# Performance work log

Hardware: AMD Instinct MI355X
Metric: run time of the kernel (lower is better)

## Reference

```python
import jax, jax.numpy as jnp
import numpy as np

NEG = -1e30  # stand-in for -inf, safe for grads


def ctc_loss(log_probs, targets, input_lengths, target_lengths):
    """PyTorch-style CTC loss, blank=0, reduction='mean'.
    log_probs: [B, T, V] log-softmaxed; targets: [B, S] (values in [1, V)).
    """
    B, T, V = log_probs.shape
    S = targets.shape[1]
    L = 2 * S + 1  # extended label seq: blank-interleaved
    ext = jnp.zeros((B, L), jnp.int32).at[:, 1::2].set(targets.astype(jnp.int32))
    prev2 = jnp.pad(ext[:, :-2], ((0, 0), (2, 0)), constant_values=-1)
    skip = (ext != 0) & (ext != prev2)  # [B, L] allow alpha[l-2] transition
    barange = jnp.arange(B)[:, None]

    # t = 0 init
    lp0e = log_probs[:, 0, :][barange, ext]  # [B, L]
    alpha0 = jnp.full((B, L), NEG, log_probs.dtype)
    alpha0 = alpha0.at[:, 0].set(lp0e[:, 0]).at[:, 1].set(lp0e[:, 1])

    def step(alpha, xs):
        t, lp_t = xs  # lp_t: [B, V]
        lpe = lp_t[barange, ext]  # [B, L]
        a1 = jnp.pad(alpha[:, :-1], ((0, 0), (1, 0)), constant_values=NEG)
        a2 = jnp.pad(alpha[:, :-2], ((0, 0), (2, 0)), constant_values=NEG)
        a2 = jnp.where(skip, a2, NEG)
        new = lpe + jnp.logaddexp(jnp.logaddexp(alpha, a1), a2)
        # freeze alpha past each sequence's length
        new = jnp.where((t < input_lengths)[:, None], new, alpha)
        return new, None

    ts = jnp.arange(1, T)
    lps = jnp.swapaxes(log_probs, 0, 1)[1:]  # [T-1, B, V]
    alpha, _ = jax.lax.scan(step, alpha0, (ts, lps))

    tl = target_lengths.astype(jnp.int32)
    brange = jnp.arange(B)
    end = alpha[brange, 2 * tl]       # trailing blank
    end2 = alpha[brange, 2 * tl - 1]  # last label
    per = -jnp.logaddexp(end, end2)
    # reduction='mean': divide each loss by its target_length, then batch mean
    return jnp.mean(per / target_lengths.astype(per.dtype))


def setup_inputs() -> dict:
    key = jax.random.key(0)
    k1, k2, k3 = jax.random.split(key, 3)
    B, T, Fd, V, S = 32, 2048, 1024, 256, 256
    features = jax.random.normal(k1, (B, T, Fd), jnp.float32)
    W = jax.random.normal(k2, (V, Fd), jnp.float32) / np.sqrt(Fd)
    b = jnp.zeros((V,), jnp.float32)
    targets = jax.random.randint(k3, (B, S), 1, V)  # avoid blank=0
    input_lengths = jnp.full((B,), T, jnp.int32)
    target_lengths = jnp.full((B,), S, jnp.int32)
    return {"features": features, "W": W, "b": b, "targets": targets,
            "input_lengths": input_lengths, "target_lengths": target_lengths}


def reference(features, W, b, targets, input_lengths, target_lengths):
    # dropout is identity at inference; classifier then log_softmax in fp32
    logits = jnp.einsum('btf,vf->btv', features, W) + b
    log_probs = jax.nn.log_softmax(logits.astype(jnp.float32), axis=-1)
    return ctc_loss(log_probs, targets, input_lengths, target_lengths)
```

## Files before the change

kernel.cpp:

```cpp
#include <hip/hip_runtime.h>
#include <hip/hip_bf16.h>

using bf16x8 = __attribute__((ext_vector_type(8))) short;
using f32x4  = __attribute__((ext_vector_type(4))) float;

constexpr int Bn = 32;
constexpr int Tn = 2048;
constexpr int Fn = 1024;
constexpr int Vn = 256;
constexpr int Sn = 256;
constexpr int Ln = 2 * Sn + 1;
constexpr int Mn = Bn * Tn;
constexpr int G2P = 272;
constexpr int DQ = 16;
constexpr int ABP = 520;

#define NEGF (-1e30f)

__device__ __forceinline__ float exp2fast(float x) { return __builtin_amdgcn_exp2f(x); }
__device__ __forceinline__ float log2fast(float x) { return __builtin_amdgcn_logf(x); }

__device__ __forceinline__ unsigned int cvt_pk_bf16(float lo, float hi) {
    unsigned int r;
    asm("v_cvt_pk_bf16_f32 %0, %1, %2" : "=v"(r) : "v"(lo), "v"(hi));
    return r;
}

__device__ __forceinline__ float lae2(float x, float y) {
    float m = fmaxf(x, y);
    float d = fminf(x, y) - m;
    return m + log2fast(1.0f + exp2fast(d));
}
__device__ __forceinline__ float lae3(float x, float y, float z) {
    float m  = fmaxf(fmaxf(x, y), z);
    float md = __builtin_amdgcn_fmed3f(x, y, z);
    float mn = fminf(fminf(x, y), z);
    return m + log2fast(1.0f + exp2fast(md - m) + exp2fast(mn - m));
}

__global__ __launch_bounds__(256) void wcvt(const float* __restrict__ W,
                                            unsigned short* __restrict__ Wb)
{
    const int idx = (blockIdx.x * 256 + threadIdx.x) * 4;
    float4 v = *reinterpret_cast<const float4*>(W + idx);
    uint2 p;
    p.x = cvt_pk_bf16(v.x, v.y);
    p.y = cvt_pk_bf16(v.z, v.w);
    *reinterpret_cast<uint2*>(Wb + idx) = p;
}

__global__ __launch_bounds__(512, 4) void gemm_ctc(
    const float* __restrict__ A,
    const unsigned short* __restrict__ Wb,
    const float* __restrict__ bias,
    const int* __restrict__ targets,
    float* __restrict__ G2)
{
    __shared__ char smem[81920];
    unsigned short* sA = (unsigned short*)smem;
    unsigned short* sB = (unsigned short*)(smem + 16384);
    float* yL    = (float*)smem;
    float* sRedA = (float*)(smem + 66048);
    float* sRedB = (float*)(smem + 68096);

    const int tid  = threadIdx.x;
    const int wid  = tid >> 6, lane = tid & 63;
    const int quad = lane >> 4, c16 = lane & 15;
    const int m0 = blockIdx.x * 128;
    const int wm = (wid & 1) * 64;
    const int wn = (wid >> 1) * 64;

    f32x4 acc[4][4] = {};

    const int arow = tid >> 2;
    const int akq  = (tid & 3) << 4;
    const float* aPtr = A + (size_t)(m0 + arow) * Fn + akq;
    const int aswz = (arow & 7) << 4;
    char* sAbase = (char*)sA + arow * 128;
    const int ab0 = (akq * 2) ^ aswz;
    const int ab1 = (akq * 2 + 16) ^ aswz;

    const int wrow8 = lane >> 3;
    const int wcol  = ((lane & 7) << 4) ^ (wrow8 << 4);

#define ISSUE_W(K0, BUF)                                                        \
    _Pragma("unroll")                                                           \
    for (int i = 0; i < 4; ++i) {                                               \
        const int rbase = wid * 32 + i * 8;                                     \
        const unsigned short* g = Wb + (size_t)(rbase + wrow8) * Fn + (K0);     \
        __builtin_amdgcn_global_load_lds(                                       \
            (const __attribute__((address_space(1))) unsigned int*)((const char*)g + wcol), \
            (__attribute__((address_space(3))) unsigned int*)((char*)sB + (BUF) * 32768 + rbase * 128), \
            16, 0, 0);                                                          \
    }

    ISSUE_W(0, 0);
    {
        const float4* ap = reinterpret_cast<const float4*>(aPtr);
        float4 av0 = ap[0], av1 = ap[1], av2 = ap[2], av3 = ap[3];
        uint4 p;
        p.x = cvt_pk_bf16(av0.x, av0.y); p.y = cvt_pk_bf16(av0.z, av0.w);
        p.z = cvt_pk_bf16(av1.x, av1.y); p.w = cvt_pk_bf16(av1.z, av1.w);
        *reinterpret_cast<uint4*>(sAbase + ab0) = p;
        p.x = cvt_pk_bf16(av2.x, av2.y); p.y = cvt_pk_bf16(av2.z, av2.w);
        p.z = cvt_pk_bf16(av3.x, av3.y); p.w = cvt_pk_bf16(av3.z, av3.w);
        *reinterpret_cast<uint4*>(sAbase + ab1) = p;
    }
    __syncthreads();

    for (int it = 0; it < 16; ++it) {
        float4 an0, an1, an2, an3;
        if (it < 15) {
            ISSUE_W((it + 1) * 64, (it + 1) & 1);
            const float4* ap = reinterpret_cast<const float4*>(aPtr + (it + 1) * 64);
            an0 = ap[0]; an1 = ap[1]; an2 = ap[2]; an3 = ap[3];
        }
        const char* sBb = (const char*)sB + (it & 1) * 32768;
        #pragma unroll
        for (int kh = 0; kh < 2; ++kh) {
            const int colq = kh * 64 + quad * 16;
            bf16x8 af[4], bf[4];
            #pragma unroll
            for (int mt = 0; mt < 4; ++mt) {
                const int r = wm + mt * 16 + c16;
                af[mt] = *reinterpret_cast<const bf16x8*>((const char*)sA + r * 128 + (colq ^ ((r & 7) << 4)));
            }
            #pragma unroll
            for (int nt = 0; nt < 4; ++nt) {
                const int r = wn + nt * 16 + c16;
                bf[nt] = *reinterpret_cast<const bf16x8*>(sBb + r * 128 + (colq ^ ((r & 7) << 4)));
            }
            #pragma unroll
            for (int mt = 0; mt < 4; ++mt)
                #pragma unroll
                for (int nt = 0; nt < 4; ++nt)
                    acc[mt][nt] = __builtin_amdgcn_mfma_f32_16x16x32_bf16(af[mt], bf[nt], acc[mt][nt], 0, 0, 0);
        }
        __syncthreads();
        if (it < 15) {
            uint4 p;
            p.x = cvt_pk_bf16(an0.x, an0.y); p.y = cvt_pk_bf16(an0.z, an0.w);
            p.z = cvt_pk_bf16(an1.x, an1.y); p.w = cvt_pk_bf16(an1.z, an1.w);
            *reinterpret_cast<uint4*>(sAbase + ab0) = p;
            p.x = cvt_pk_bf16(an2.x, an2.y); p.y = cvt_pk_bf16(an2.z, an2.w);
            p.z = cvt_pk_bf16(an3.x, an3.y); p.w = cvt_pk_bf16(an3.z, an3.w);
            *reinterpret_cast<uint4*>(sAbase + ab1) = p;
            __syncthreads();
        }
    }
#undef ISSUE_W

    const float L2E = 1.4426950408889634f;
    const int wng = wid >> 1;

    float bv[4];
    #pragma unroll
    for (int nt = 0; nt < 4; ++nt) bv[nt] = bias[wn + nt * 16 + c16];
    #pragma unroll
    for (int mt = 0; mt < 4; ++mt)
        #pragma unroll
        for (int nt = 0; nt < 4; ++nt)
            #pragma unroll
            for (int r = 0; r < 4; ++r)
                acc[mt][nt][r] += bv[nt];

    float rmx[4][4];
    #pragma unroll
    for (int mt = 0; mt < 4; ++mt)
        #pragma unroll
        for (int r = 0; r < 4; ++r) {
            float m = fmaxf(fmaxf(acc[mt][0][r], acc[mt][1][r]),
                            fmaxf(acc[mt][2][r], acc[mt][3][r]));
            #pragma unroll
            for (int off = 8; off >= 1; off >>= 1) m = fmaxf(m, __shfl_xor(m, off, 64));
            rmx[mt][r] = m;
        }
    __syncthreads();
    if (c16 == 0) {
        #pragma unroll
        for (int mt = 0; mt < 4; ++mt)
            #pragma unroll
            for (int r = 0; r < 4; ++r)
                sRedA[(wm + mt * 16 + quad * 4 + r) * 4 + wng] = rmx[mt][r];
    }
    __syncthreads();

    float mL[4][4], sm[4][4];
    #pragma unroll
    for (int mt = 0; mt < 4; ++mt)
        #pragma unroll
        for (int r = 0; r < 4; ++r) {
            const int row = wm + mt * 16 + quad * 4 + r;
            float4 mp = ((const float4*)sRedA)[row];
            mL[mt][r] = fmaxf(fmaxf(mp.x, mp.y), fmaxf(mp.z, mp.w)) * L2E;
            float s = 0.0f;
            #pragma unroll
            for (int nt = 0; nt < 4; ++nt)
                s += exp2fast(fmaf(acc[mt][nt][r], L2E, -mL[mt][r]));
            #pragma unroll
            for (int off = 8; off >= 1; off >>= 1) s += __shfl_xor(s, off, 64);
            sm[mt][r] = s;
        }
    if (c16 == 0) {
        #pragma unroll
        for (int mt = 0; mt < 4; ++mt)
            #pragma unroll
            for (int r = 0; r < 4; ++r)
                sRedB[(wm + mt * 16 + quad * 4 + r) * 4 + wng] = sm[mt][r];
    }
    __syncthreads();

    float cr[4][4];
    #pragma unroll
    for (int mt = 0; mt < 4; ++mt)
        #pragma unroll
        for (int r = 0; r < 4; ++r) {
            const int row = wm + mt * 16 + quad * 4 + r;
            float4 sp = ((const float4*)sRedB)[row];
            cr[mt][r] = -(mL[mt][r] + log2fast((sp.x + sp.y) + (sp.z + sp.w)));
        }

    const int* tg = targets + (m0 >> 11) * Sn;
    int tgc[5];
    #pragma unroll
    for (int k = 0; k < 5; ++k) {
        const int c = lane + (k << 6);
        tgc[k] = (c == 0) ? 0 : ((c < 257) ? tg[c - 1] : 0);
    }

    #pragma unroll
    for (int h = 0; h < 2; ++h) {
        if ((wid & 1) == h) {
            #pragma unroll
            for (int mt = 0; mt < 4; ++mt)
                #pragma unroll
                for (int nt = 0; nt < 4; ++nt)
                    #pragma unroll
                    for (int r = 0; r < 4; ++r)
                        yL[(mt * 16 + quad * 4 + r) * 258 + wn + nt * 16 + c16] =
                            fmaf(acc[mt][nt][r], L2E, cr[mt][r]);
        }
        __syncthreads();
        #pragma unroll
        for (int rr = 0; rr < 8; ++rr) {
            const int row = wid * 8 + rr;
            const float* yrow = yL + row * 258;
            float vals[5];
            #pragma unroll
            for (int k = 0; k < 5; ++k) vals[k] = yrow[tgc[k]];
            float* gout = G2 + (size_t)(m0 + h * 64 + row) * G2P;
            #pragma unroll
            for (int k = 0; k < 4; ++k) gout[lane + (k << 6)] = vals[k];
            if (lane == 0) gout[256] = vals[4];
        }
        __syncthreads();
    }
}

__global__ __launch_bounds__(512) void ctc_fb(
    const float* __restrict__ G2, const int* __restrict__ targets,
    const int* __restrict__ ilen, const int* __restrict__ tlen,
    float* __restrict__ abuf)
{
    const int blk = blockIdx.x;
    const bool bwd = blk >= Bn;
    const int b = bwd ? blk - Bn : blk;
    const int tid = threadIdx.x;
    const int w = tid >> 6, j = tid & 63;
    __shared__ float sAl[Ln];
    const float* __restrict__ Gb = G2 + (size_t)b * Tn * G2P;
    const int* tg = targets + b * Sn;
    const int len = ilen[b];
    const int tl  = tlen[b];
    float* outp = abuf + (size_t)(bwd ? Bn + b : b) * ABP;
    const int NEGI = __float_as_int(NEGF);

    if (!bwd) {
        const int own_lo = (w == 0) ? 0 : 64 * w + 2;
        const int own_hi = min(64 * w + 66, Ln);
        const int lbase  = 64 * w - 62 + 2 * j;
        const int l0 = lbase, l1 = lbase + 1;
        const int s_c = min(max(32 * w - 31 + j, 0), Sn - 1);

        const bool own0 = (l0 >= own_lo) && (l0 < own_hi);
        const bool own1 = (l1 >= own_lo) && (l1 < own_hi);
        const bool re0  = (l0 >= 0) && (l0 < Ln) && !own0;
        const bool re1  = (l1 >= 0) && (l1 < Ln) && !own1;
        bool sk1 = false;
        if (l1 >= 1 && l1 < Ln) { int s = l1 >> 1; sk1 = (s == 0) || (tg[s] != tg[s - 1]); }

        float a0, a1;
        {
            float bl0 = Gb[0];
            float od0 = Gb[1 + s_c];
            a0 = (l0 == 0) ? bl0 : NEGF;
            a1 = (l1 == 1) ? od0 : NEGF;
        }
        if (own0) sAl[l0] = a0;
        if (own1) sAl[l1] = a1;
        __syncthreads();
        if (re0) a0 = sAl[l0];
        if (re1) a1 = sAl[l1];
        __syncthreads();

        unsigned oB = G2P, oO = G2P + 1 + s_c;
        float plB[DQ], plO[DQ];
        #pragma unroll
        for (int d = 0; d < DQ; ++d) {
            plB[d] = Gb[oB]; plO[d] = Gb[oO];
            oB += G2P; oO += G2P;
        }

        int t = 1;
        for (int chunk = 0; chunk < 32; ++chunk) {
            #pragma unroll
            for (int kk = 0; kk < 32; ++kk, ++t) {
                const int pidx = kk & (DQ - 1);
                float gb = plB[pidx], go = plO[pidx];
                plB[pidx] = Gb[oB]; plO[pidx] = Gb[oO];
                oB += G2P; oO += G2P;
                float p = __int_as_float(__builtin_amdgcn_update_dpp(
                    NEGI, __float_as_int(a1), 0x138, 0xf, 0xf, false));
                if (t < len) {
                    float z  = sk1 ? p : NEGF;
                    float n0 = gb + lae2(a0, p);
                    float n1 = go + lae3(a1, a0, z);
                    a0 = n0; a1 = n1;
                }
            }
            if (own0) sAl[l0] = a0;
            if (own1) sAl[l1] = a1;
            __syncthreads();
            if (re0) a0 = sAl[l0];
            if (re1) a1 = sAl[l1];
            __syncthreads();
        }
        if (own0) outp[l0] = a0;
        if (own1) outp[l1] = a1;
    } else {
        const int l0 = 64 * w + 2 * j;
        const int l1 = l0 + 1;
        const int s  = 32 * w + j;
        const int s_c = min(s, Sn - 1);
        const bool act0 = l0 < Ln, act1 = l1 < Ln;
        const bool own0 = act0 && ((j < 32) || (l0 == Ln - 1));
        const bool own1 = act1 && (j < 32);
        const bool re0 = act0 && !own0, re1 = act1 && !own1;
        bool skb = false;
        if (s + 1 < Sn) skb = (tg[s + 1] != tg[s]);

        float a0 = (act0 && l0 == 2 * tl)     ? 0.0f : NEGF;
        float a1 = (act1 && l1 == 2 * tl - 1) ? 0.0f : NEGF;
        if (own0) sAl[l0] = a0;
        if (own1) sAl[l1] = a1;
        __syncthreads();
        if (re0) a0 = sAl[l0];
        if (re1) a1 = sAl[l1];
        __syncthreads();

        unsigned oB = (unsigned)Tn * G2P;
        unsigned oO = oB + 1 + s_c;
        float plB[DQ], plO[DQ];
        #pragma unroll
        for (int d = 0; d < DQ; ++d) {
            plB[d] = Gb[oB]; plO[d] = Gb[oO];
            oB -= G2P; oO -= G2P;
        }

        int tt = Tn;
        for (int chunk = 0; chunk < 32; ++chunk) {
            #pragma unroll
            for (int kk = 0; kk < 32; ++kk, --tt) {
                const int pidx = kk & (DQ - 1);
                float gb = plB[pidx], go = plO[pidx];
                plB[pidx] = Gb[oB]; plO[pidx] = Gb[oO];
                oB -= G2P; oO -= G2P;
                if (tt < len) {
                    float c0 = gb + a0;
                    float c1 = go + a1;
                    float d0 = __int_as_float(__builtin_amdgcn_update_dpp(
                        NEGI, __float_as_int(c0), 0x130, 0xf, 0xf, false));
                    float d1 = __int_as_float(__builtin_amdgcn_update_dpp(
                        NEGI, __float_as_int(c1), 0x130, 0xf, 0xf, false));
                    a0 = lae2(c0, c1);
                    a1 = lae3(c1, d0, skb ? d1 : NEGF);
                }
            }
            if (own0) sAl[l0] = a0;
            if (own1) sAl[l1] = a1;
            __syncthreads();
            if (re0) a0 = sAl[l0];
            if (re1) a1 = sAl[l1];
            __syncthreads();
        }
        if (own0) outp[l0] = a0;
        if (own1) outp[l1] = a1;
    }
}

__global__ __launch_bounds__(64) void ctc_combine(
    const float* __restrict__ abuf, const int* __restrict__ tlen,
    float* __restrict__ loss_b)
{
    const int b = blockIdx.x, lane = threadIdx.x;
    const float* ap = abuf + (size_t)b * ABP;
    const float* bp = abuf + (size_t)(Bn + b) * ABP;
    float x[9];
    #pragma unroll
    for (int k = 0; k < 9; ++k) {
        const int l = lane + (k << 6);
        x[k] = (l < Ln) ? (ap[l] + bp[l]) : NEGF;
    }
    float m = x[0];
    #pragma unroll
    for (int k = 1; k < 9; ++k) m = fmaxf(m, x[k]);
    #pragma unroll
    for (int off = 32; off >= 1; off >>= 1) m = fmaxf(m, __shfl_xor(m, off, 64));
    float s = 0.0f;
    #pragma unroll
    for (int k = 0; k < 9; ++k) s += exp2fast(x[k] - m);
    #pragma unroll
    for (int off = 32; off >= 1; off >>= 1) s += __shfl_xor(s, off, 64);
    if (lane == 0)
        loss_b[b] = -0.6931471805599453f * (m + log2fast(s)) / (float)tlen[b];
}

__global__ void final_reduce(const float* __restrict__ loss_b, float* __restrict__ out)
{
    const int lane = threadIdx.x;
    float v = (lane < Bn) ? loss_b[lane] : 0.0f;
    #pragma unroll
    for (int off = 32; off >= 1; off >>= 1) v += __shfl_xor(v, off, 64);
    if (lane == 0) out[0] = v * (1.0f / Bn);
}

extern "C" void kernel_launch(void* const* d_in, const int* in_sizes, int n_in,
                              void* d_out, int out_size, void* d_ws, size_t ws_size,
                              hipStream_t stream) {
    const float* feat = (const float*)d_in[0];
    const float* W    = (const float*)d_in[1];
    const float* bias = (const float*)d_in[2];
    const int* tgt    = (const int*)d_in[3];
    const int* il     = (const int*)d_in[4];
    const int* tl     = (const int*)d_in[5];
    float* out = (float*)d_out;

    char* ws = (char*)d_ws;
    float* G2 = (float*)ws;
    size_t g2b = (size_t)Mn * G2P * sizeof(float) + 32768;
    unsigned short* Wb = (unsigned short*)(ws + g2b);
    float* abuf  = (float*)(ws + g2b + (size_t)Vn * Fn * sizeof(unsigned short));
    float* lossb = abuf + 2 * Bn * ABP;

    wcvt<<<(Vn * Fn) / 1024, 256, 0, stream>>>(W, Wb);
    gemm_ctc<<<Mn / 128, 512, 0, stream>>>(feat, Wb, bias, tgt, G2);
    ctc_fb<<<2 * Bn, 512, 0, stream>>>(G2, tgt, il, tl, abuf);
    ctc_combine<<<Bn, 64, 0, stream>>>(abuf, tl, lossb);
    final_reduce<<<1, 64, 0, stream>>>(lossb, out);
}
```

Baseline: 564.4 us.

## Deepen GEMM prefetch to two stages with manual waitcnt and barriers

Result: no change. 562.1 us (-0.4%).

```diff
diff --git a/kernel.cpp b/kernel.cpp
--- a/kernel.cpp
+++ b/kernel.cpp
@@ -94,28 +94,40 @@
             16, 0, 0);                                                          \
     }
 
+#define LOAD_A(DST, K0) {                                                       \
+        const float4* ap = reinterpret_cast<const float4*>(aPtr + (K0));        \
+        DST[0] = ap[0]; DST[1] = ap[1]; DST[2] = ap[2]; DST[3] = ap[3]; }
+
+#define STORE_A(av) { uint4 p;                                                  \
+        p.x = cvt_pk_bf16(av[0].x, av[0].y); p.y = cvt_pk_bf16(av[0].z, av[0].w); \
+        p.z = cvt_pk_bf16(av[1].x, av[1].y); p.w = cvt_pk_bf16(av[1].z, av[1].w); \
+        *reinterpret_cast<uint4*>(sAbase + ab0) = p;                            \
+        p.x = cvt_pk_bf16(av[2].x, av[2].y); p.y = cvt_pk_bf16(av[2].z, av[2].w); \
+        p.z = cvt_pk_bf16(av[3].x, av[3].y); p.w = cvt_pk_bf16(av[3].z, av[3].w); \
+        *reinterpret_cast<uint4*>(sAbase + ab1) = p; }
+
+#define FENCE() asm volatile("" ::: "memory")
+#define BARRIER() { FENCE(); __builtin_amdgcn_s_barrier(); FENCE(); }
+
+    float4 apre[2][4];
+
+    LOAD_A(apre[0], 0);
+    __builtin_amdgcn_sched_barrier(0);
     ISSUE_W(0, 0);
-    {
-        const float4* ap = reinterpret_cast<const float4*>(aPtr);
-        float4 av0 = ap[0], av1 = ap[1], av2 = ap[2], av3 = ap[3];
-        uint4 p;
-        p.x = cvt_pk_bf16(av0.x, av0.y); p.y = cvt_pk_bf16(av0.z, av0.w);
-        p.z = cvt_pk_bf16(av1.x, av1.y); p.w = cvt_pk_bf16(av1.z, av1.w);
-        *reinterpret_cast<uint4*>(sAbase + ab0) = p;
-        p.x = cvt_pk_bf16(av2.x, av2.y); p.y = cvt_pk_bf16(av2.z, av2.w);
-        p.z = cvt_pk_bf16(av3.x, av3.y); p.w = cvt_pk_bf16(av3.z, av3.w);
-        *reinterpret_cast<uint4*>(sAbase + ab1) = p;
-    }
-    __syncthreads();
-
-    for (int it = 0; it < 16; ++it) {
-        float4 an0, an1, an2, an3;
-        if (it < 15) {
-            ISSUE_W((it + 1) * 64, (it + 1) & 1);
-            const float4* ap = reinterpret_cast<const float4*>(aPtr + (it + 1) * 64);
-            an0 = ap[0]; an1 = ap[1]; an2 = ap[2]; an3 = ap[3];
-        }
-        const char* sBb = (const char*)sB + (it & 1) * 32768;
+    __builtin_amdgcn_sched_barrier(0);
+    STORE_A(apre[0]);
+    LOAD_A(apre[1], 64);
+    __builtin_amdgcn_sched_barrier(0);
+    ISSUE_W(64, 1);
+    __builtin_amdgcn_sched_barrier(0);
+    asm volatile("s_waitcnt vmcnt(8)" ::: "memory");
+    asm volatile("s_waitcnt lgkmcnt(0)" ::: "memory");
+    __builtin_amdgcn_sched_barrier(0);
+    BARRIER();
+
+    #pragma unroll
+    for (int k = 0; k < 16; ++k) {
+        const char* sBb = (const char*)sB + (k & 1) * 32768;
         #pragma unroll
         for (int kh = 0; kh < 2; ++kh) {
             const int colq = kh * 64 + quad * 16;
@@ -136,19 +148,28 @@
                 for (int nt = 0; nt < 4; ++nt)
                     acc[mt][nt] = __builtin_amdgcn_mfma_f32_16x16x32_bf16(af[mt], bf[nt], acc[mt][nt], 0, 0, 0);
         }
-        __syncthreads();
-        if (it < 15) {
-            uint4 p;
-            p.x = cvt_pk_bf16(an0.x, an0.y); p.y = cvt_pk_bf16(an0.z, an0.w);
-            p.z = cvt_pk_bf16(an1.x, an1.y); p.w = cvt_pk_bf16(an1.z, an1.w);
-            *reinterpret_cast<uint4*>(sAbase + ab0) = p;
-            p.x = cvt_pk_bf16(an2.x, an2.y); p.y = cvt_pk_bf16(an2.z, an2.w);
-            p.z = cvt_pk_bf16(an3.x, an3.y); p.w = cvt_pk_bf16(an3.z, an3.w);
-            *reinterpret_cast<uint4*>(sAbase + ab1) = p;
-            __syncthreads();
+        asm volatile("s_waitcnt lgkmcnt(0)" ::: "memory");
+        __builtin_amdgcn_sched_barrier(0);
+        BARRIER();
+
+        if (k < 15) {
+            if (k < 14) {
+                LOAD_A(apre[k & 1], (k + 2) * 64);
+                __builtin_amdgcn_sched_barrier(0);
+                ISSUE_W((k + 2) * 64, k & 1);
+                __builtin_amdgcn_sched_barrier(0);
+            }
+            STORE_A(apre[(k + 1) & 1]);
+            if (k < 14) { asm volatile("s_waitcnt vmcnt(8)" ::: "memory"); }
+            else        { asm volatile("s_waitcnt vmcnt(0)" ::: "memory"); }
+            asm volatile("s_waitcnt lgkmcnt(0)" ::: "memory");
+            __builtin_amdgcn_sched_barrier(0);
+            BARRIER();
         }
     }
 #undef ISSUE_W
+#undef LOAD_A
+#undef STORE_A
 
     const float L2E = 1.4426950408889634f;
     const int wng = wid >> 1;
@@ -303,12 +324,13 @@
         if (re1) a1 = sAl[l1];
         __syncthreads();
 
-        unsigned oB = G2P, oO = G2P + 1 + s_c;
-        float plB[DQ], plO[DQ];
+        size_t rOB = G2P;
+        unsigned oO = G2P + 1 + s_c;
+        float sgb[DQ], plO[DQ];
         #pragma unroll
         for (int d = 0; d < DQ; ++d) {
-            plB[d] = Gb[oB]; plO[d] = Gb[oO];
-            oB += G2P; oO += G2P;
+            sgb[d] = Gb[rOB]; plO[d] = Gb[oO];
+            rOB += G2P; oO += G2P;
         }
 
         int t = 1;
@@ -316,9 +338,9 @@
             #pragma unroll
             for (int kk = 0; kk < 32; ++kk, ++t) {
                 const int pidx = kk & (DQ - 1);
-                float gb = plB[pidx], go = plO[pidx];
-                plB[pidx] = Gb[oB]; plO[pidx] = Gb[oO];
-                oB += G2P; oO += G2P;
+                float gb = sgb[pidx], go = plO[pidx];
+                sgb[pidx] = Gb[rOB]; plO[pidx] = Gb[oO];
+                rOB += G2P; oO += G2P;
                 float p = __int_as_float(__builtin_amdgcn_update_dpp(
                     NEGI, __float_as_int(a1), 0x138, 0xf, 0xf, false));
                 if (t < len) {
@@ -358,13 +380,13 @@
         if (re1) a1 = sAl[l1];
         __syncthreads();
 
-        unsigned oB = (unsigned)Tn * G2P;
-        unsigned oO = oB + 1 + s_c;
-        float plB[DQ], plO[DQ];
+        size_t rOB = (size_t)Tn * G2P;
+        unsigned oO = (unsigned)rOB + 1 + s_c;
+        float sgb[DQ], plO[DQ];
         #pragma unroll
         for (int d = 0; d < DQ; ++d) {
-            plB[d] = Gb[oB]; plO[d] = Gb[oO];
-            oB -= G2P; oO -= G2P;
+            sgb[d] = Gb[rOB]; plO[d] = Gb[oO];
+            rOB -= G2P; oO -= G2P;
         }
 
         int tt = Tn;
@@ -372,9 +394,9 @@
             #pragma unroll
             for (int kk = 0; kk < 32; ++kk, --tt) {
                 const int pidx = kk & (DQ - 1);
-                float gb = plB[pidx], go = plO[pidx];
-                plB[pidx] = Gb[oB]; plO[pidx] = Gb[oO];
-                oB -= G2P; oO -= G2P;
+                float gb = sgb[pidx], go = plO[pidx];
+                sgb[pidx] = Gb[rOB]; plO[pidx] = Gb[oO];
+                rOB -= G2P; oO -= G2P;
                 if (tt < len) {
                     float c0 = gb + a0;
                     float c1 = go + a1;
```
